# Performance work log

Measured on AMD Instinct MI355X. Metric: run time of the kernel, lower is better.

The kernel has to match this reference:

```python
import jax, jax.numpy as jnp
import numpy as np

N_USER = 300000
M_ITEM = 700000
DIM = 64
LAYERS = 3
DROPOUT = 0.1
N_EDGES = 1200000
BATCH = 4096
N_NODES = N_USER + M_ITEM


def setup_inputs() -> dict:
    key = jax.random.key(0)
    ks = jax.random.split(key, 7)
    user_emb = jax.random.normal(ks[0], (N_USER, DIM), dtype=jnp.float32) * 0.1
    item_emb = jax.random.normal(ks[1], (M_ITEM, DIM), dtype=jnp.float32) * 0.1
    edge_src = jax.random.randint(ks[2], (N_EDGES,), 0, N_NODES)
    edge_dst = jax.random.randint(ks[3], (N_EDGES,), 0, N_NODES)
    # symmetric-normalized adjacency values are small positives; uniform suffices
    edge_vals = jax.random.uniform(ks[4], (N_EDGES,), dtype=jnp.float32)
    users = jax.random.randint(ks[5], (BATCH,), 0, N_USER)
    items = jax.random.randint(ks[6], (BATCH,), 0, M_ITEM)
    return {
        "user_emb": user_emb,
        "item_emb": item_emb,
        "edge_vals": edge_vals,
        "edge_src": edge_src,
        "edge_dst": edge_dst,
        "users": users,
        "items": items,
    }


def reference(user_emb, item_emb, edge_vals, edge_src, edge_dst, users, items):
    n_user = user_emb.shape[0]
    # train-mode edge dropout: drop with prob DROPOUT, rescale kept values.
    # Dropped edges are zeroed (equivalent to removal under SpMM).
    keep = jax.random.uniform(jax.random.key(42), (edge_vals.shape[0],)) >= DROPOUT
    vals = jnp.where(keep, edge_vals / (1.0 - DROPOUT), 0.0)

    all_emb = jnp.concatenate([user_emb, item_emb], axis=0)  # [N, D]
    embs = [all_emb]
    for _ in range(LAYERS):
        msg = vals[:, None] * all_emb[edge_src]  # [E, D] gather + scale
        all_emb = jax.ops.segment_sum(msg, edge_dst, num_segments=N_NODES)
        embs.append(all_emb)
    stacked = jnp.stack(embs, axis=1)  # [N, L+1, D]
    light = jnp.mean(stacked, axis=1)  # [N, D] mean layer pooling

    u_final = light[:n_user][users]      # [B, D]
    i_final = light[n_user:][items]      # [B, D]
    inter = u_final * i_final            # [B, D]
    ratings = jax.nn.sigmoid(jnp.sum(inter, axis=1))  # [B]

    # per-layer interactions: [B, L+1, D]
    inter_layers = stacked[:n_user][users] * stacked[n_user:][items]
    return ratings, inter, inter_layers
```

## Files before the change

kernel.cpp:

```cpp
#include <hip/hip_runtime.h>

#define N_USER   300000
#define M_ITEM   700000
#define N_NODES  (N_USER + M_ITEM)
#define DIM      64
#define N_EDGES  1200000
#define BATCH    4096

__device__ __forceinline__ unsigned rotl32(unsigned x, int r) {
    return (x << r) | (x >> (32 - r));
}

__device__ __forceinline__ float edge_veff(int e, float val) {
    unsigned ks[3] = {0u, 42u, 0u ^ 42u ^ 0x1BD11BDAu};
    unsigned x0 = ks[0];
    unsigned x1 = (unsigned)e + ks[1];
    const int rotA[4] = {13, 15, 26, 6};
    const int rotB[4] = {17, 29, 16, 24};
#pragma unroll
    for (int g = 0; g < 5; ++g) {
#pragma unroll
        for (int j = 0; j < 4; ++j) {
            int r = (g & 1) ? rotB[j] : rotA[j];
            x0 += x1;
            x1 = rotl32(x1, r);
            x1 ^= x0;
        }
        x0 += ks[(g + 1) % 3];
        x1 += ks[(g + 2) % 3] + (unsigned)(g + 1);
    }
    unsigned bits = x0 ^ x1;
    float u = __uint_as_float((bits >> 9) | 0x3F800000u) - 1.0f;
    return (u >= 0.1f) ? val * (1.0f / 0.9f) : 0.0f;
}

__global__ void fill_kernel(int4* __restrict__ head4) {
    const int TOT4 = N_NODES / 4;
    int tid = blockIdx.x * blockDim.x + threadIdx.x;
    int stride = gridDim.x * blockDim.x;
    int4 m1 = make_int4(-1, -1, -1, -1);
    for (int i = tid; i < TOT4; i += stride) head4[i] = m1;
}

__global__ void push_kernel(const int* __restrict__ edst,
                            const float* __restrict__ evals,
                            int* __restrict__ head,
                            int* __restrict__ nxt,
                            float* __restrict__ val) {
    int e = blockIdx.x * blockDim.x + threadIdx.x;
    if (e >= N_EDGES) return;
    float v = edge_veff(e, evals[e]);
    if (v == 0.0f) return;
    val[e] = v;
    nxt[e] = atomicExch(&head[edst[e]], e);
}

__device__ __forceinline__ float emb0(const float* __restrict__ ue,
                                      const float* __restrict__ ie, int s, int d) {
    return (s < N_USER) ? ue[(size_t)s * DIM + d] : ie[(size_t)(s - N_USER) * DIM + d];
}

__device__ __forceinline__ void pull3(int n, int d,
                                      const float* __restrict__ ue,
                                      const float* __restrict__ ie,
                                      const int* __restrict__ head,
                                      const int* __restrict__ nxt,
                                      const float* __restrict__ val,
                                      const int* __restrict__ esrc,
                                      float& u1, float& u2, float& u3) {
    u1 = 0.f; u2 = 0.f; u3 = 0.f;
    for (int e1 = head[n]; e1 != -1; e1 = nxt[e1]) {
        float v1 = val[e1];
        int s1 = esrc[e1];
        u1 += v1 * emb0(ue, ie, s1, d);
        float a1 = 0.f, a2 = 0.f;
        for (int e2 = head[s1]; e2 != -1; e2 = nxt[e2]) {
            float v2 = val[e2];
            int s2 = esrc[e2];
            a1 += v2 * emb0(ue, ie, s2, d);
            float b1 = 0.f;
            for (int e3 = head[s2]; e3 != -1; e3 = nxt[e3]) {
                b1 += val[e3] * emb0(ue, ie, esrc[e3], d);
            }
            a2 += v2 * b1;
        }
        u2 += v1 * a1;
        u3 += v1 * a2;
    }
}

__global__ void out_kernel(const float* __restrict__ user_emb,
                           const float* __restrict__ item_emb,
                           const int* __restrict__ users,
                           const int* __restrict__ items,
                           const int* __restrict__ head,
                           const int* __restrict__ nxt,
                           const float* __restrict__ val,
                           const int* __restrict__ esrc,
                           float* __restrict__ ratings,
                           float* __restrict__ inter,
                           float* __restrict__ inter_layers) {
    int gt = blockIdx.x * blockDim.x + threadIdx.x;
    int b = gt >> 6, d = gt & 63;
    if (b >= BATCH) return;
    int un = users[b];
    int in_node = N_USER + items[b];

    float u0 = user_emb[(size_t)un * DIM + d];
    float i0 = item_emb[(size_t)items[b] * DIM + d];
    float u1, u2, u3, i1, i2, i3;
    pull3(un, d, user_emb, item_emb, head, nxt, val, esrc, u1, u2, u3);
    pull3(in_node, d, user_emb, item_emb, head, nxt, val, esrc, i1, i2, i3);

    size_t base = (size_t)b * 4 * DIM + d;
    inter_layers[base + 0 * DIM] = u0 * i0;
    inter_layers[base + 1 * DIM] = u1 * i1;
    inter_layers[base + 2 * DIM] = u2 * i2;
    inter_layers[base + 3 * DIM] = u3 * i3;

    float lu = (u0 + u1 + u2 + u3) * 0.25f;
    float li = (i0 + i1 + i2 + i3) * 0.25f;
    float p = lu * li;
    inter[(size_t)b * DIM + d] = p;
    float s = p;
#pragma unroll
    for (int off = 32; off > 0; off >>= 1) s += __shfl_down(s, off, 64);
    if (d == 0) ratings[b] = 1.0f / (1.0f + expf(-s));
}

extern "C" void kernel_launch(void* const* d_in, const int* in_sizes, int n_in,
                              void* d_out, int out_size, void* d_ws, size_t ws_size,
                              hipStream_t stream) {
    const float* user_emb  = (const float*)d_in[0];
    const float* item_emb  = (const float*)d_in[1];
    const float* edge_vals = (const float*)d_in[2];
    const int*   edge_src  = (const int*)d_in[3];
    const int*   edge_dst  = (const int*)d_in[4];
    const int*   users     = (const int*)d_in[5];
    const int*   items     = (const int*)d_in[6];

    float* out          = (float*)d_out;
    float* ratings      = out;
    float* inter        = out + BATCH;
    float* inter_layers = out + BATCH + BATCH * DIM;

    char* ws = (char*)d_ws;
    size_t off = 0;
    int* head = (int*)(ws + off); off += (size_t)N_NODES * sizeof(int);
    int* nxt  = (int*)(ws + off); off += (size_t)N_EDGES * sizeof(int);
    float* val = (float*)(ws + off); off += (size_t)N_EDGES * sizeof(float);

    const dim3 blk(256);

    fill_kernel<<<512, blk, 0, stream>>>((int4*)head);
    push_kernel<<<(N_EDGES + 255) / 256, blk, 0, stream>>>(
        edge_dst, edge_vals, head, nxt, val);
    out_kernel<<<(BATCH * 64 + 255) / 256, blk, 0, stream>>>(
        user_emb, item_emb, users, items, head, nxt, val, edge_src,
        ratings, inter, inter_layers);
}
```

Before: 82.89 us.

## Pack edge list nodes into int4 and split user/item pulls across wavefronts

The separate nxt/val/esrc arrays become one packed int4 record per edge, written in the push kernel, so each linked-list hop needs a single 16-byte load instead of three dependent scattered loads. The output kernel also gives the user and item traversals to separate wavefronts and exchanges the results through shared memory. This doubles the wave-level parallelism of the latency-bound pointer chasing. The cost is a larger per-edge workspace, wider writes in the push kernel, and a block barrier.

```diff
diff --git a/kernel.cpp b/kernel.cpp
--- a/kernel.cpp
+++ b/kernel.cpp
@@ -42,17 +42,17 @@
     for (int i = tid; i < TOT4; i += stride) head4[i] = m1;
 }
 
-__global__ void push_kernel(const int* __restrict__ edst,
+__global__ void push_kernel(const int* __restrict__ esrc,
+                            const int* __restrict__ edst,
                             const float* __restrict__ evals,
                             int* __restrict__ head,
-                            int* __restrict__ nxt,
-                            float* __restrict__ val) {
+                            int4* __restrict__ node) {
     int e = blockIdx.x * blockDim.x + threadIdx.x;
     if (e >= N_EDGES) return;
     float v = edge_veff(e, evals[e]);
     if (v == 0.0f) return;
-    val[e] = v;
-    nxt[e] = atomicExch(&head[edst[e]], e);
+    int old = atomicExch(&head[edst[e]], e);
+    node[e] = make_int4(old, esrc[e], __float_as_int(v), 0);
 }
 
 __device__ __forceinline__ float emb0(const float* __restrict__ ue,
@@ -64,23 +64,27 @@
                                       const float* __restrict__ ue,
                                       const float* __restrict__ ie,
                                       const int* __restrict__ head,
-                                      const int* __restrict__ nxt,
-                                      const float* __restrict__ val,
-                                      const int* __restrict__ esrc,
+                                      const int4* __restrict__ node,
                                       float& u1, float& u2, float& u3) {
     u1 = 0.f; u2 = 0.f; u3 = 0.f;
-    for (int e1 = head[n]; e1 != -1; e1 = nxt[e1]) {
-        float v1 = val[e1];
-        int s1 = esrc[e1];
+    for (int e1 = head[n]; e1 != -1; ) {
+        int4 n1 = node[e1];
+        e1 = n1.x;
+        int s1 = n1.y;
+        float v1 = __int_as_float(n1.z);
         u1 += v1 * emb0(ue, ie, s1, d);
         float a1 = 0.f, a2 = 0.f;
-        for (int e2 = head[s1]; e2 != -1; e2 = nxt[e2]) {
-            float v2 = val[e2];
-            int s2 = esrc[e2];
+        for (int e2 = head[s1]; e2 != -1; ) {
+            int4 n2 = node[e2];
+            e2 = n2.x;
+            int s2 = n2.y;
+            float v2 = __int_as_float(n2.z);
             a1 += v2 * emb0(ue, ie, s2, d);
             float b1 = 0.f;
-            for (int e3 = head[s2]; e3 != -1; e3 = nxt[e3]) {
-                b1 += val[e3] * emb0(ue, ie, esrc[e3], d);
+            for (int e3 = head[s2]; e3 != -1; ) {
+                int4 n3 = node[e3];
+                e3 = n3.x;
+                b1 += __int_as_float(n3.z) * emb0(ue, ie, n3.y, d);
             }
             a2 += v2 * b1;
         }
@@ -94,38 +98,48 @@
                            const int* __restrict__ users,
                            const int* __restrict__ items,
                            const int* __restrict__ head,
-                           const int* __restrict__ nxt,
-                           const float* __restrict__ val,
-                           const int* __restrict__ esrc,
+                           const int4* __restrict__ node,
                            float* __restrict__ ratings,
                            float* __restrict__ inter,
                            float* __restrict__ inter_layers) {
-    int gt = blockIdx.x * blockDim.x + threadIdx.x;
-    int b = gt >> 6, d = gt & 63;
-    if (b >= BATCH) return;
-    int un = users[b];
-    int in_node = N_USER + items[b];
+    __shared__ float sh[4][4][DIM];
+    int w = threadIdx.x >> 6;
+    int d = threadIdx.x & 63;
+    int b = blockIdx.x * 2 + (w >> 1);
+    bool is_item = (w & 1);
 
-    float u0 = user_emb[(size_t)un * DIM + d];
-    float i0 = item_emb[(size_t)items[b] * DIM + d];
-    float u1, u2, u3, i1, i2, i3;
-    pull3(un, d, user_emb, item_emb, head, nxt, val, esrc, u1, u2, u3);
-    pull3(in_node, d, user_emb, item_emb, head, nxt, val, esrc, i1, i2, i3);
+    int root = is_item ? (N_USER + items[b]) : users[b];
+    float x0 = emb0(user_emb, item_emb, root, d);
+    float x1, x2, x3;
+    pull3(root, d, user_emb, item_emb, head, node, x1, x2, x3);
 
-    size_t base = (size_t)b * 4 * DIM + d;
-    inter_layers[base + 0 * DIM] = u0 * i0;
-    inter_layers[base + 1 * DIM] = u1 * i1;
-    inter_layers[base + 2 * DIM] = u2 * i2;
-    inter_layers[base + 3 * DIM] = u3 * i3;
+    sh[w][0][d] = x0;
+    sh[w][1][d] = x1;
+    sh[w][2][d] = x2;
+    sh[w][3][d] = x3;
+    __syncthreads();
 
-    float lu = (u0 + u1 + u2 + u3) * 0.25f;
-    float li = (i0 + i1 + i2 + i3) * 0.25f;
-    float p = lu * li;
-    inter[(size_t)b * DIM + d] = p;
-    float s = p;
+    if (!is_item) {
+        float i0 = sh[w + 1][0][d];
+        float i1 = sh[w + 1][1][d];
+        float i2 = sh[w + 1][2][d];
+        float i3 = sh[w + 1][3][d];
+
+        size_t base = (size_t)b * 4 * DIM + d;
+        inter_layers[base + 0 * DIM] = x0 * i0;
+        inter_layers[base + 1 * DIM] = x1 * i1;
+        inter_layers[base + 2 * DIM] = x2 * i2;
+        inter_layers[base + 3 * DIM] = x3 * i3;
+
+        float lu = (x0 + x1 + x2 + x3) * 0.25f;
+        float li = (i0 + i1 + i2 + i3) * 0.25f;
+        float p = lu * li;
+        inter[(size_t)b * DIM + d] = p;
+        float s = p;
 #pragma unroll
-    for (int off = 32; off > 0; off >>= 1) s += __shfl_down(s, off, 64);
-    if (d == 0) ratings[b] = 1.0f / (1.0f + expf(-s));
+        for (int off = 32; off > 0; off >>= 1) s += __shfl_down(s, off, 64);
+        if (d == 0) ratings[b] = 1.0f / (1.0f + expf(-s));
+    }
 }
 
 extern "C" void kernel_launch(void* const* d_in, const int* in_sizes, int n_in,
@@ -147,15 +161,14 @@
     char* ws = (char*)d_ws;
     size_t off = 0;
     int* head = (int*)(ws + off); off += (size_t)N_NODES * sizeof(int);
-    int* nxt  = (int*)(ws + off); off += (size_t)N_EDGES * sizeof(int);
-    float* val = (float*)(ws + off); off += (size_t)N_EDGES * sizeof(float);
+    int4* node = (int4*)(ws + off); off += (size_t)N_EDGES * sizeof(int4);
 
     const dim3 blk(256);
 
     fill_kernel<<<512, blk, 0, stream>>>((int4*)head);
     push_kernel<<<(N_EDGES + 255) / 256, blk, 0, stream>>>(
-        edge_dst, edge_vals, head, nxt, val);
-    out_kernel<<<(BATCH * 64 + 255) / 256, blk, 0, stream>>>(
-        user_emb, item_emb, users, items, head, nxt, val, edge_src,
+        edge_src, edge_dst, edge_vals, head, (int4*)node);
+    out_kernel<<<BATCH / 2, blk, 0, stream>>>(
+        user_emb, item_emb, users, items, head, node,
         ratings, inter, inter_layers);
 }
```

Result: faster. 79.87 us (median of 2 runs) (-3.6%).
